# Kernel optimization log

Hardware: AMD Instinct MI355X
Metric: run time of the kernel (lower is better)

Reference implementation:

```python
import jax, jax.numpy as jnp
import numpy as np

BS, EP = 32, 32
N_AGENTS, N_ATOM, EMBED = 8, 51, 32
STATE_DIM, HYP = 128, 64
V_MIN, V_MAX = -10.0, 10.0


def proj(support, probs, v_min, v_max, n_atom):
    # C51 categorical projection of (support, probs) onto the fixed atom grid
    # linspace(v_min, v_max, n_atom). support/probs: [..., M] -> [..., n_atom]
    support, probs = jnp.broadcast_arrays(support, probs)
    delta = (v_max - v_min) / (n_atom - 1)
    b = (jnp.clip(support, v_min, v_max) - v_min) / delta
    l = jnp.floor(b)
    u = jnp.ceil(b)
    eq = (u == l).astype(probs.dtype)  # support exactly on an atom -> all mass to l
    ml = probs * (u - b + eq)
    mu = probs * (b - l)
    shp = probs.shape
    n = int(np.prod(shp[:-1]))
    m = shp[-1]
    rows = jnp.arange(n)[:, None]
    out = jnp.zeros((n, n_atom), probs.dtype)
    out = out.at[rows, l.astype(jnp.int32).reshape(n, m)].add(ml.reshape(n, m))
    out = out.at[rows, u.astype(jnp.int32).reshape(n, m)].add(mu.reshape(n, m))
    return out.reshape(shp[:-1] + (n_atom,))


def bconv(p, q):
    # Full 1D convolution of per-row categorical pmfs (sum of two random vars).
    # p: [N, L], q: [N, M] -> [N, L+M-1], via grouped conv (one group per row).
    N, L = p.shape
    M = q.shape[-1]
    out = jax.lax.conv_general_dilated(
        p[None], jnp.flip(q, -1)[:, None, :],
        window_strides=(1,), padding=[(M - 1, M - 1)],
        feature_group_count=N, dimension_numbers=('NCW', 'OIW', 'NCW'))
    return out[0]


def mlp2(x, w1, b1, w2, b2):
    return jax.nn.relu(x @ w1.T + b1) @ w2.T + b2


def setup_inputs():
    key = jax.random.key(0)
    ks = jax.random.split(key, 20)
    def p(k, shape, s=0.05):
        return jax.random.normal(k, shape, dtype=jnp.float32) * s
    aq = jax.random.uniform(ks[0], (BS, EP, N_AGENTS, N_ATOM), dtype=jnp.float32)
    aq = aq / jnp.sum(aq, -1, keepdims=True)  # valid categorical distributions
    return {
        'agent_qs_distri': aq,
        'states': p(ks[1], (BS, EP, STATE_DIM), 1.0),
        'hw1_w1': p(ks[2], (HYP, STATE_DIM)), 'hw1_b1': p(ks[3], (HYP,)),
        'hw1_w2': p(ks[4], (EMBED * N_AGENTS, HYP)), 'hw1_b2': p(ks[5], (EMBED * N_AGENTS,)),
        'hb1_w': p(ks[6], (EMBED, STATE_DIM)), 'hb1_b': p(ks[7], (EMBED,)),
        'hwf_w1': p(ks[8], (HYP, STATE_DIM)), 'hwf_b1': p(ks[9], (HYP,)),
        'hwf_w2': p(ks[10], (EMBED, HYP)), 'hwf_b2': p(ks[11], (EMBED,)),
        'v_w1': p(ks[12], (EMBED, STATE_DIM)), 'v_b1': p(ks[13], (EMBED,)),
        'v_w2': p(ks[14], (1, EMBED)), 'v_b2': p(ks[15], (1,)),
    }


def reference(agent_qs_distri, states, hw1_w1, hw1_b1, hw1_w2, hw1_b2,
              hb1_w, hb1_b, hwf_w1, hwf_b1, hwf_w2, hwf_b2,
              v_w1, v_b1, v_w2, v_b2):
    bs, ep, n_agents, n_atom = agent_qs_distri.shape
    s = states.reshape(-1, STATE_DIM)
    atoms = jnp.linspace(V_MIN, V_MAX, n_atom).astype(jnp.float32)  # [A]

    w1 = jnp.abs(mlp2(s, hw1_w1, hw1_b1, hw1_w2, hw1_b2)).reshape(bs, ep, EMBED, n_agents)
    b1 = (s @ hb1_w.T + hb1_b).reshape(bs, ep, EMBED)

    # stage 1: scale each agent's support by w1[..., k, i], project back onto atoms
    sup1 = atoms * w1[..., None]                                       # [bs,ep,E,Na,A]
    aw = proj(sup1, agent_qs_distri[:, :, None], V_MIN, V_MAX, n_atom)  # [bs,ep,E,Na,A]
    awf = aw.reshape(-1, n_agents, n_atom)                              # [bs*ep*E,Na,A]
    q = awf[:, 0]
    for i in range(1, n_agents):
        q = bconv(q, awf[:, i])                                         # [.., Na*A-Na+1]
    L1 = n_agents * n_atom - n_agents + 1
    sup = jnp.linspace(n_agents * V_MIN, n_agents * V_MAX, L1).astype(jnp.float32)
    sup = jax.nn.elu(sup + b1[..., None])                               # [bs,ep,E,L1]
    x = proj(sup, q.reshape(bs, ep, EMBED, L1), V_MIN, V_MAX, n_atom)   # [bs,ep,E,A]

    # stage 2: hyper_w_final scaling, convolve across embed dim, add V(s)
    wf = jnp.abs(mlp2(s, hwf_w1, hwf_b1, hwf_w2, hwf_b2)).reshape(bs, ep, EMBED)
    xw = proj(atoms * wf[..., None], x, V_MIN, V_MAX, n_atom)           # [bs,ep,E,A]
    xwf = xw.reshape(-1, EMBED, n_atom)
    q = xwf[:, 0]
    for i in range(1, EMBED):
        q = bconv(q, xwf[:, i])                                         # [bs*ep, E*A-E+1]
    L2 = EMBED * n_atom - EMBED + 1
    v = mlp2(s, v_w1, v_b1, v_w2, v_b2).reshape(bs, ep, 1)
    sup2 = jnp.linspace(EMBED * V_MIN, EMBED * V_MAX, L2).astype(jnp.float32) + v
    return proj(sup2, q.reshape(bs, ep, L2), V_MIN, V_MAX, n_atom)      # [bs,ep,A]
```

## Files before the change

kernel.cpp:

```cpp
#include <hip/hip_runtime.h>
#include <hip/hip_bf16.h>
#include <math.h>

typedef unsigned short u16;

#define WAVE_SYNC() asm volatile("s_waitcnt lgkmcnt(0)" ::: "memory")

__device__ __forceinline__ float bf2f(u16 u) {
  union { unsigned int i; float f; } c;
  c.i = ((unsigned int)u) << 16;
  return c.f;
}
__device__ __forceinline__ float bflo(unsigned int u) {
  union { unsigned int i; float f; } c; c.i = u << 16; return c.f;
}
__device__ __forceinline__ float bfhi(unsigned int u) {
  union { unsigned int i; float f; } c; c.i = u & 0xffff0000u; return c.f;
}
__device__ __forceinline__ u16 f2bf(float f) {
  union { float f; unsigned int i; } c;
  c.f = f;
  unsigned int x = c.i;
  unsigned int r = (x + 0x7fffu + ((x >> 16) & 1u)) >> 16;
  return (u16)r;
}

__device__ __forceinline__ void proj_bounds(float wv, int& ML, int& MH) {
  float smin = (-10.0f + 0.4f * 0.0f)  * wv;
  float smax = (-10.0f + 0.4f * 50.0f) * wv;
  float bmin = (fminf(fmaxf(smin, -10.0f), 10.0f) + 10.0f) / 0.4f;
  float bmax = (fminf(fmaxf(smax, -10.0f), 10.0f) + 10.0f) / 0.4f;
  ML = (int)floorf(bmin);
  MH = (int)ceilf(bmax);
}

template<typename SUPP>
__device__ __forceinline__ void proj_scan(float* __restrict__ g1,
                                          float* __restrict__ g2,
                                          int span, int lane, SUPP supp)
{
  if (lane < 52) g1[lane] = 0.f;
  if (lane < 53) g2[lane] = 0.f;
  float cml = 0.f, cmu = 0.f;
  int ck = -1;
  for (int base = 0; base < span; base += 64) {
    int t = base + lane;
    bool act = (t < span);
    int tc = act ? t : (span - 1);
    float sup, p;
    supp(tc, act, sup, p);
    float c  = fminf(fmaxf(sup, -10.0f), 10.0f);
    float b  = (c + 10.0f) / 0.4f;
    float l  = floorf(b);
    float u  = ceilf(b);
    float eq = (u == l) ? 1.0f : 0.0f;
    float ml = p * (u - b + eq);
    float mu = p * (b - l);
    int   li = (int)l;
    bool last = (base + 64 >= span);
    if (lane == 0 && ck >= 0) {
      if (ck == li) { ml += cml; mu += cmu; }
      else          { g1[ck] = cml; g2[ck + 1] = cmu; }
    }
#pragma unroll
    for (int d = 1; d < 64; d <<= 1) {
      int   lo = __shfl_up(li, d);
      float a1 = __shfl_up(ml, d);
      float a2 = __shfl_up(mu, d);
      bool same = (lane >= d) && (lo == li);
      ml += same ? a1 : 0.f;
      mu += same ? a2 : 0.f;
    }
    int ln = __shfl_down(li, 1);
    bool runend = (lane == 63) ? last : (ln != li);
    if (runend) { g1[li] = ml; g2[li + 1] = mu; }
    if (!last) {
      cml = __shfl(ml, 63);
      cmu = __shfl(mu, 63);
      ck  = __shfl(li, 63);
    }
  }
}

__device__ __forceinline__ void conv_pad2(const float* __restrict__ q,
                                          float* __restrict__ qn,
                                          const float* __restrict__ kvs,
                                          int ML, int W, int T,
                                          int LQ, int HQ, int tid, int nthr)
{
  const int Lout = LQ + ML, Hout = HQ + ML + T;
  for (int J = Lout + tid; J <= Hout; J += nthr) {
    const float* qp = q + (J - ML);
    float acc = 0.f;
    for (int c = 0; c < W; c += 4) {
      float4 k4 = *(const float4*)(kvs + c);
      acc = fmaf(k4.x, qp[-c],     acc);
      acc = fmaf(k4.y, qp[-c - 1], acc);
      acc = fmaf(k4.z, qp[-c - 2], acc);
      acc = fmaf(k4.w, qp[-c - 3], acc);
    }
    qn[J] = acc;
  }
}

template<int BF>
__device__ __forceinline__ float ldt(const void* p, int i) {
  if (BF) return bf2f(((const u16*)p)[i]);
  return ((const float*)p)[i];
}

template<int BF>
__device__ __forceinline__ float dot128_t(const void* w, int row, const float* s) {
  float acc = 0.f;
  if (BF) {
    const uint4* p = (const uint4*)((const u16*)w + row * 128);
#pragma unroll
    for (int i = 0; i < 16; ++i) {
      uint4 v = p[i];
      int b = i * 8;
      acc = fmaf(bflo(v.x), s[b + 0], acc); acc = fmaf(bfhi(v.x), s[b + 1], acc);
      acc = fmaf(bflo(v.y), s[b + 2], acc); acc = fmaf(bfhi(v.y), s[b + 3], acc);
      acc = fmaf(bflo(v.z), s[b + 4], acc); acc = fmaf(bfhi(v.z), s[b + 5], acc);
      acc = fmaf(bflo(v.w), s[b + 6], acc); acc = fmaf(bfhi(v.w), s[b + 7], acc);
    }
  } else {
    const float4* p = (const float4*)((const float*)w + row * 128);
#pragma unroll
    for (int i = 0; i < 32; ++i) {
      float4 v = p[i];
      int b = i * 4;
      acc = fmaf(v.x, s[b + 0], acc); acc = fmaf(v.y, s[b + 1], acc);
      acc = fmaf(v.z, s[b + 2], acc); acc = fmaf(v.w, s[b + 3], acc);
    }
  }
  return acc;
}

template<int BF>
__device__ __forceinline__ float dot64_t(const void* w, int row, const float* h) {
  float acc = 0.f;
  if (BF) {
    const uint4* p = (const uint4*)((const u16*)w + row * 64);
#pragma unroll
    for (int i = 0; i < 8; ++i) {
      uint4 v = p[i];
      int b = i * 8;
      acc = fmaf(bflo(v.x), h[b + 0], acc); acc = fmaf(bfhi(v.x), h[b + 1], acc);
      acc = fmaf(bflo(v.y), h[b + 2], acc); acc = fmaf(bfhi(v.y), h[b + 3], acc);
      acc = fmaf(bflo(v.z), h[b + 4], acc); acc = fmaf(bfhi(v.z), h[b + 5], acc);
      acc = fmaf(bflo(v.w), h[b + 6], acc); acc = fmaf(bfhi(v.w), h[b + 7], acc);
    }
  } else {
    const float4* p = (const float4*)((const float*)w + row * 64);
#pragma unroll
    for (int i = 0; i < 16; ++i) {
      float4 v = p[i];
      int b = i * 4;
      acc = fmaf(v.x, h[b + 0], acc); acc = fmaf(v.y, h[b + 1], acc);
      acc = fmaf(v.z, h[b + 2], acc); acc = fmaf(v.w, h[b + 3], acc);
    }
  }
  return acc;
}

template<int BF>
__device__ __forceinline__ void mlp_body(
    const void* states,
    const void* hw1_w1, const void* hw1_b1, const void* hw1_w2, const void* hw1_b2,
    const void* hb1_w,  const void* hb1_b,
    const void* hwf_w1, const void* hwf_b1, const void* hwf_w2, const void* hwf_b2,
    const void* v_w1,   const void* v_b1,   const void* v_w2,   const void* v_b2,
    float* w1_ws, float* b1_ws, float* wf_ws, float* v_ws,
    int n, int tid, float* s, float* h1, float* hf, float* vh)
{
  s[tid]      = ldt<BF>(states, n * 128 + tid);
  s[tid + 64] = ldt<BF>(states, n * 128 + 64 + tid);
  __syncthreads();

  h1[tid] = fmaxf(dot128_t<BF>(hw1_w1, tid, s) + ldt<BF>(hw1_b1, tid), 0.f);
  hf[tid] = fmaxf(dot128_t<BF>(hwf_w1, tid, s) + ldt<BF>(hwf_b1, tid), 0.f);
  if (tid < 32) {
    vh[tid] = fmaxf(dot128_t<BF>(v_w1, tid, s) + ldt<BF>(v_b1, tid), 0.f);
    b1_ws[n * 32 + tid] = dot128_t<BF>(hb1_w, tid, s) + ldt<BF>(hb1_b, tid);
  }
  __syncthreads();

#pragma unroll
  for (int k = 0; k < 4; ++k) {
    int o = tid + 64 * k;
    w1_ws[n * 256 + o] = fabsf(dot64_t<BF>(hw1_w2, o, h1) + ldt<BF>(hw1_b2, o));
  }
  if (tid < 32)
    wf_ws[n * 32 + tid] = fabsf(dot64_t<BF>(hwf_w2, tid, hf) + ldt<BF>(hwf_b2, tid));
  if (tid == 0) {
    float acc = ldt<BF>(v_b2, 0);
    for (int e = 0; e < 32; ++e) acc = fmaf(ldt<BF>(v_w2, e), vh[e], acc);
    v_ws[n] = acc;
  }
}

__global__ __launch_bounds__(64) void k_mlp(
    const void* __restrict__ states,
    const void* __restrict__ hw1_w1, const void* __restrict__ hw1_b1,
    const void* __restrict__ hw1_w2, const void* __restrict__ hw1_b2,
    const void* __restrict__ hb1_w,  const void* __restrict__ hb1_b,
    const void* __restrict__ hwf_w1, const void* __restrict__ hwf_b1,
    const void* __restrict__ hwf_w2, const void* __restrict__ hwf_b2,
    const void* __restrict__ v_w1,   const void* __restrict__ v_b1,
    const void* __restrict__ v_w2,   const void* __restrict__ v_b2,
    float* __restrict__ w1_ws, float* __restrict__ b1_ws,
    float* __restrict__ wf_ws, float* __restrict__ v_ws,
    int* __restrict__ flag)
{
  __shared__ float s[128];
  __shared__ float h1[64];
  __shared__ float hf[64];
  __shared__ float vh[32];
  const int n = blockIdx.x;
  const int tid = threadIdx.x;

  const u16* sr = (const u16*)states;
  unsigned int e0 = (sr[tid] >> 7) & 0xFF;
  unsigned int e1 = (sr[tid + 64] >> 7) & 0xFF;
  unsigned long long bl0 = __ballot(e0 >= 97 && e0 <= 141);
  unsigned long long bl1 = __ballot(e1 >= 97 && e1 <= 141);
  int bf = (__popcll(bl0) + __popcll(bl1) >= 104) ? 1 : 0;
  if (tid == 0) *flag = bf;

  if (bf)
    mlp_body<1>(states, hw1_w1, hw1_b1, hw1_w2, hw1_b2, hb1_w, hb1_b,
                hwf_w1, hwf_b1, hwf_w2, hwf_b2, v_w1, v_b1, v_w2, v_b2,
                w1_ws, b1_ws, wf_ws, v_ws, n, tid, s, h1, hf, vh);
  else
    mlp_body<0>(states, hw1_w1, hw1_b1, hw1_w2, hw1_b2, hb1_w, hb1_b,
                hwf_w1, hwf_b1, hwf_w2, hwf_b2, v_w1, v_b1, v_w2, v_b2,
                w1_ws, b1_ws, wf_ws, v_ws, n, tid, s, h1, hf, vh);
}

__global__ __launch_bounds__(128) void k_perembed(
    const void* __restrict__ aq,
    const float* __restrict__ w1_ws, const float* __restrict__ b1_ws,
    const float* __restrict__ wf_ws, float* __restrict__ xw_ws,
    const int* __restrict__ flag)
{
  __shared__ __align__(16) float Ab[2][520];
  __shared__ __align__(16) float Bb[2][520];
  __shared__ __align__(16) float kvsb[2][56];
  __shared__ float gAb[2][53];
  __shared__ float gBb[2][54];

  const int w    = threadIdx.x >> 6;
  const int lane = threadIdx.x & 63;
  const int task = blockIdx.x * 2 + w;
  const int n = task >> 5;
  const int e = task & 31;
  const int bf = *flag;

  float* A   = Ab[w];
  float* B   = Bb[w];
  float* kvs = kvsb[w];
  float* gA  = gAb[w];
  float* gB  = gBb[w];

  float pv[8];
  if (bf) {
    const u16* p = (const u16*)aq + n * 408 + lane;
#pragma unroll
    for (int a = 0; a < 8; ++a) pv[a] = (lane < 51) ? bf2f(p[a * 51]) : 0.f;
  } else {
    const float* p = (const float*)aq + n * 408 + lane;
#pragma unroll
    for (int a = 0; a < 8; ++a) pv[a] = (lane < 51) ? p[a * 51] : 0.f;
  }
  float wreg = (lane < 8) ? w1_ws[n * 256 + e * 8 + lane] : 0.f;
  float b1v  = b1_ws[n * 32 + e];
  float wfv  = wf_ws[n * 32 + e];

  float wv0 = __shfl(wreg, 0);
  int ML0, MH0;
  proj_bounds(wv0, ML0, MH0);
  {
    float pa = pv[0];
    proj_scan(gA, gB, 51, lane, [&](int t, bool act, float& sup, float& p) {
      sup = (-10.0f + 0.4f * (float)t) * wv0;
      p = act ? pa : 0.f;
    });
  }
  if (lane <= MH0 - ML0)
    A[64 + ML0 + lane] = gA[ML0 + lane] + gB[ML0 + lane];
  WAVE_SYNC();

  int LQ = 64 + ML0, HQ = 64 + MH0;
  float* q = A;
  float* qn = B;
#pragma unroll
  for (int a = 1; a < 8; ++a) {
    float wv = __shfl(wreg, a);
    int ML, MH;
    proj_bounds(wv, ML, MH);
    int T = MH - ML;
    int W = (T + 4) & ~3;
    float pa = pv[a];
    proj_scan(gA, gB, 51, lane, [&](int t, bool act, float& sup, float& p) {
      sup = (-10.0f + 0.4f * (float)t) * wv;
      p = act ? pa : 0.f;
    });
    if (lane < W)     kvs[lane] = (lane <= T) ? (gA[ML + lane] + gB[ML + lane]) : 0.f;
    if (lane < W - 1) q[LQ - 1 - lane] = 0.f;
    if (lane < T)     q[HQ + 1 + lane] = 0.f;
    WAVE_SYNC();
    conv_pad2(q, qn, kvs, ML, W, T, LQ, HQ, lane, 64);
    WAVE_SYNC();
    LQ += ML; HQ += MH;
    float* t_ = q; q = qn; qn = t_;
  }

  {
    int span = HQ - LQ + 1;
    int LQl = LQ;
    const float* qf = q;
    proj_scan(gA, gB, span, lane, [&](int t, bool act, float& sup, float& p) {
      int tg = (LQl - 64) + t;
      float raw = (-80.0f + 0.4f * (float)tg) + b1v;
      sup = (raw > 0.f) ? raw : expm1f(raw);
      p = act ? qf[LQl + t] : 0.f;
    });
  }
  WAVE_SYNC();

  float x2v = (lane < 51) ? (gA[lane] + gB[lane]) : 0.f;
  WAVE_SYNC();
  int MLf, MHf;
  proj_bounds(wfv, MLf, MHf);
  proj_scan(gA, gB, 51, lane, [&](int t, bool act, float& sup, float& p) {
    sup = (-10.0f + 0.4f * (float)t) * wfv;
    p = act ? x2v : 0.f;
  });
  WAVE_SYNC();
  if (lane <= MHf - MLf)
    xw_ws[task * 51 + MLf + lane] = gA[MLf + lane] + gB[MLf + lane];
}

__global__ __launch_bounds__(256) void k_final(
    const float* __restrict__ xw_ws, const float* __restrict__ wf_ws,
    const float* __restrict__ v_ws,
    void* __restrict__ out, const int* __restrict__ flag)
{
  __shared__ __align__(16) float A[1720];
  __shared__ __align__(16) float B[1720];
  __shared__ __align__(16) float kvs[56];
  __shared__ float gA[53];
  __shared__ float gB[54];

  const int n    = blockIdx.x;
  const int tid  = threadIdx.x;
  const int lane = tid & 63;
  const int bf   = *flag;

  float wfreg = (lane < 32) ? wf_ws[n * 32 + lane] : 0.f;
  float vv    = v_ws[n];

  float wv0 = __shfl(wfreg, 0);
  int ML0, MH0;
  proj_bounds(wv0, ML0, MH0);
  if (tid <= MH0 - ML0)
    A[64 + ML0 + tid] = xw_ws[(n * 32 + 0) * 51 + ML0 + tid];

  int LQ = 64 + ML0, HQ = 64 + MH0;
  float* q = A;
  float* qn = B;

  int MLn, MHn;
  { float wvn = __shfl(wfreg, 1); proj_bounds(wvn, MLn, MHn); }
  float nv = (tid <= MHn - MLn) ? xw_ws[(n * 32 + 1) * 51 + MLn + tid] : 0.f;

  for (int e = 1; e < 32; ++e) {
    int ML = MLn, MH = MHn;
    int T = MH - ML;
    int W = (T + 4) & ~3;
    if (tid < W)     kvs[tid] = (tid <= T) ? nv : 0.f;
    if (tid < W - 1) q[LQ - 1 - tid] = 0.f;
    if (tid < T)     q[HQ + 1 + tid] = 0.f;
    if (e < 31) {
      float wvn = __shfl(wfreg, e + 1);
      proj_bounds(wvn, MLn, MHn);
      nv = (tid <= MHn - MLn) ? xw_ws[(n * 32 + e + 1) * 51 + MLn + tid] : 0.f;
    }
    __syncthreads();
    conv_pad2(q, qn, kvs, ML, W, T, LQ, HQ, tid, 256);
    __syncthreads();
    LQ += ML; HQ += MH;
    float* t_ = q; q = qn; qn = t_;
  }

  if (tid < 64) {
    int span = HQ - LQ + 1;
    int LQl = LQ;
    const float* qf = q;
    proj_scan(gA, gB, span, lane, [&](int t, bool act, float& sup, float& p) {
      int tg = (LQl - 64) + t;
      sup = (-320.0f + 0.4f * (float)tg) + vv;
      p = act ? qf[LQl + t] : 0.f;
    });
  }
  __syncthreads();

  if (tid < 51) {
    float o = gA[tid] + gB[tid];
    if (bf) ((u16*)out)[n * 51 + tid] = f2bf(o);
    else    ((float*)out)[n * 51 + tid] = o;
  }
}

extern "C" void kernel_launch(void* const* d_in, const int* in_sizes, int n_in,
                              void* d_out, int out_size, void* d_ws, size_t ws_size,
                              hipStream_t stream)
{
  float* ws    = (float*)d_ws;
  float* w1_ws = ws;
  float* b1_ws = w1_ws + 1024 * 256;
  float* wf_ws = b1_ws + 1024 * 32;
  float* v_ws  = wf_ws + 1024 * 32;
  float* xw_ws = v_ws  + 1024;
  int*   flag  = (int*)(xw_ws + 1024 * 32 * 51);

  k_mlp<<<1024, 64, 0, stream>>>(d_in[1],
      d_in[2], d_in[3], d_in[4], d_in[5], d_in[6], d_in[7],
      d_in[8], d_in[9], d_in[10], d_in[11], d_in[12], d_in[13],
      d_in[14], d_in[15],
      w1_ws, b1_ws, wf_ws, v_ws, flag);

  k_perembed<<<16384, 128, 0, stream>>>(d_in[0], w1_ws, b1_ws, wf_ws, xw_ws, flag);

  k_final<<<1024, 256, 0, stream>>>(xw_ws, wf_ws, v_ws, d_out, flag);
}
```

Before: 250.7 us.

## Replace sequential 32-way convolution chain with pairwise tree reduction in k_final

The final kernel used to convolve the 32 embedding pmfs one after another, which took 31 dependent steps separated by barriers. It now computes each row's trimmed length and a packed shared-memory layout up front, loads all rows at once, and convolves them pairwise in a 5-level tree. The tree does more arithmetic at the upper levels, since both operands are long, but it needs only 5 barrier-separated stages and keeps all threads busy. In exchange it uses much more LDS (two 4608-float buffers) and adds zero-padding bookkeeping, which may lower occupancy.

Result: no change. 250.0 us (-0.3%).

```diff
diff --git a/kernel.cpp b/kernel.cpp
--- a/kernel.cpp
+++ b/kernel.cpp
@@ -346,11 +346,14 @@
     const float* __restrict__ v_ws,
     void* __restrict__ out, const int* __restrict__ flag)
 {
-  __shared__ __align__(16) float A[1720];
-  __shared__ __align__(16) float B[1720];
-  __shared__ __align__(16) float kvs[56];
-  __shared__ float gA[53];
-  __shared__ float gB[54];
+  __shared__ __align__(16) float bufA[4608];
+  __shared__ __align__(16) float bufB[4608];
+  __shared__ int meta_s[63];
+  __shared__ int meta_l[63];
+  __shared__ int meta_ml[32];
+  __shared__ int meta_g[6];
+  __shared__ int meta_mltot;
+  __shared__ float gA[53], gB[54];
 
   const int n    = blockIdx.x;
   const int tid  = threadIdx.x;
@@ -360,55 +363,120 @@
   float wfreg = (lane < 32) ? wf_ws[n * 32 + lane] : 0.f;
   float vv    = v_ws[n];
 
-  float wv0 = __shfl(wfreg, 0);
-  int ML0, MH0;
-  proj_bounds(wv0, ML0, MH0);
-  if (tid <= MH0 - ML0)
-    A[64 + ML0 + tid] = xw_ws[(n * 32 + 0) * 51 + ML0 + tid];
-
-  int LQ = 64 + ML0, HQ = 64 + MH0;
-  float* q = A;
-  float* qn = B;
-
-  int MLn, MHn;
-  { float wvn = __shfl(wfreg, 1); proj_bounds(wvn, MLn, MHn); }
-  float nv = (tid <= MHn - MLn) ? xw_ws[(n * 32 + 1) * 51 + MLn + tid] : 0.f;
-
-  for (int e = 1; e < 32; ++e) {
-    int ML = MLn, MH = MHn;
-    int T = MH - ML;
-    int W = (T + 4) & ~3;
-    if (tid < W)     kvs[tid] = (tid <= T) ? nv : 0.f;
-    if (tid < W - 1) q[LQ - 1 - tid] = 0.f;
-    if (tid < T)     q[HQ + 1 + tid] = 0.f;
-    if (e < 31) {
-      float wvn = __shfl(wfreg, e + 1);
-      proj_bounds(wvn, MLn, MHn);
-      nv = (tid <= MHn - MLn) ? xw_ws[(n * 32 + e + 1) * 51 + MLn + tid] : 0.f;
+  for (int i = tid; i < 4608; i += 256) { bufA[i] = 0.f; bufB[i] = 0.f; }
+
+  if (tid < 64) {
+    int ml, mh;
+    proj_bounds(wfreg, ml, mh);
+    if (lane < 32) meta_ml[lane] = ml;
+    int msum = ml;
+#pragma unroll
+    for (int d = 1; d < 32; d <<= 1) msum += __shfl_xor(msum, d);
+    if (lane == 0) meta_mltot = msum;
+
+    int curlen = mh - ml + 1;
+    int base = 0, Ncur = 32;
+#pragma unroll
+    for (int c = 0; c <= 5; ++c) {
+      int lm = (lane < Ncur) ? curlen : 0;
+#pragma unroll
+      for (int d = 1; d < 32; d <<= 1) {
+        int o = __shfl_xor(lm, d);
+        lm = (o > lm) ? o : lm;
+      }
+      int G = (lm + 11) & ~3;
+      int sp = ((curlen + 3) & ~3) + G;
+      int inc = (lane < Ncur) ? sp : 0;
+      int v0 = inc;
+#pragma unroll
+      for (int d = 1; d < 32; d <<= 1) {
+        int u = __shfl_up(inc, d);
+        if (lane >= d && lane < 32) inc += u;
+      }
+      if (lane < Ncur) {
+        meta_s[base + lane] = 832 + (inc - v0);
+        meta_l[base + lane] = curlen;
+      }
+      if (lane == 0) meta_g[c] = G;
+      if (c < 5) {
+        int l0 = __shfl(curlen, 2 * lane);
+        int l1 = __shfl(curlen, 2 * lane + 1);
+        curlen = l0 + l1 - 1;
+        base += Ncur;
+        Ncur >>= 1;
+      }
+    }
+  }
+  __syncthreads();
+
+  {
+    int g = tid >> 3, i = tid & 7;
+    int s = meta_s[g], l = meta_l[g], ml = meta_ml[g];
+    const float* row = xw_ws + (n * 32 + g) * 51 + ml;
+    for (int i0 = i; i0 < l; i0 += 8) bufA[s + i0] = row[i0];
+  }
+  __syncthreads();
+
+#pragma unroll
+  for (int c = 1; c <= 5; ++c) {
+    const float* bin = (c & 1) ? bufA : bufB;
+    float*       bout = (c & 1) ? bufB : bufA;
+    const int Nout = 32 >> c;
+    const int lg = 3 + c;
+    const int gs = 1 << lg;
+    const int k  = tid >> lg;
+    const int st = tid & (gs - 1);
+    const int bc = 64 - (64 >> c);
+    const int bp = 64 - (64 >> (c - 1));
+    const int i0 = bp + 2 * k;
+    const int sA = meta_s[i0];
+    const int sB = meta_s[i0 + 1];
+    const int lB = meta_l[i0 + 1];
+    const int sO = meta_s[bc + k];
+    const int lO = meta_l[bc + k];
+    const int W  = (lB + 3) & ~3;
+
+    for (int j = st * 2; j < lO; j += gs * 2) {
+      const float* Ap = bin + sA + j + 1;
+      float a0 = 0.f, a1 = 0.f;
+      for (int m = 0; m < W; m += 4) {
+        float4 k4 = *(const float4*)(bin + sB + m);
+        float v0 = Ap[-m], v1 = Ap[-m - 1], v2 = Ap[-m - 2];
+        float v3 = Ap[-m - 3], v4 = Ap[-m - 4];
+        a0 = fmaf(k4.x, v1, fmaf(k4.y, v2, fmaf(k4.z, v3, fmaf(k4.w, v4, a0))));
+        a1 = fmaf(k4.x, v0, fmaf(k4.y, v1, fmaf(k4.z, v2, fmaf(k4.w, v3, a1))));
+      }
+      bout[sO + j] = a0;
+      if (j + 1 < lO) bout[sO + j + 1] = a1;
+    }
+
+    if (c >= 2 && c <= 4) {
+      int G = meta_g[c];
+      for (int p = tid; p < G; p += 256) bout[832 - G + p] = 0.f;
+      for (int k2 = 0; k2 < Nout; ++k2) {
+        int ss = meta_s[bc + k2] + meta_l[bc + k2];
+        int ee = (k2 + 1 < Nout) ? meta_s[bc + k2 + 1]
+                                 : ss + G + 3;
+        for (int p = ss + tid; p < ee; p += 256) bout[p] = 0.f;
+      }
     }
     __syncthreads();
-    conv_pad2(q, qn, kvs, ML, W, T, LQ, HQ, tid, 256);
-    __syncthreads();
-    LQ += ML; HQ += MH;
-    float* t_ = q; q = qn; qn = t_;
   }
 
   if (tid < 64) {
-    int span = HQ - LQ + 1;
-    int LQl = LQ;
-    const float* qf = q;
-    proj_scan(gA, gB, span, lane, [&](int t, bool act, float& sup, float& p) {
-      int tg = (LQl - 64) + t;
+    int s5 = meta_s[62], l5 = meta_l[62], mlt = meta_mltot;
+    const float* qf = bufB + s5;
+    proj_scan(gA, gB, l5, lane, [&](int t, bool act, float& sup, float& p) {
+      int tg = mlt + t;
       sup = (-320.0f + 0.4f * (float)tg) + vv;
-      p = act ? qf[LQl + t] : 0.f;
+      p = act ? qf[t] : 0.f;
     });
-  }
-  __syncthreads();
-
-  if (tid < 51) {
-    float o = gA[tid] + gB[tid];
-    if (bf) ((u16*)out)[n * 51 + tid] = f2bf(o);
-    else    ((float*)out)[n * 51 + tid] = o;
+    WAVE_SYNC();
+    if (lane < 51) {
+      float o = gA[lane] + gB[lane];
+      if (bf) ((u16*)out)[n * 51 + lane] = f2bf(o);
+      else    ((float*)out)[n * 51 + lane] = o;
+    }
   }
 }
 
```
